# Performance work log

Hardware: AMD Instinct MI355X
Metric: run time of the kernel (lower is better)

## Reference

```python
import jax, jax.numpy as jnp
import numpy as np

N = 20000      # nodes
E = 320000     # edges (before self loops)
G = 128        # graphs
V = 128        # node-type vocab (VOCAB_SIZE)
DE = 64        # node_emb_dim
H = 4          # heads
C = 128        # hidden_dim per head
D = H * C      # 512, per-layer width
OUT = 256      # output_dim
EPS_LN = 1e-5
NEG_SLOPE = 0.2


def _glorot(k, shape):
    fan_in, fan_out = shape[0], shape[-1]
    s = jnp.sqrt(2.0 / (fan_in + fan_out))
    return jax.random.normal(k, shape, dtype=jnp.float32) * s


def setup_inputs() -> dict:
    key = jax.random.key(0)
    ks = jax.random.split(key, 40)
    inp = {}
    inp['node_ids'] = jax.random.randint(ks[0], (N,), 0, V)
    inp['edge_index'] = jax.random.randint(ks[1], (2, E), 0, N)
    inp['batch_vec'] = jnp.sort(jax.random.randint(ks[2], (N,), 0, G))
    emb = _glorot(ks[3], (V, DE))
    inp['emb'] = emb.at[0].set(0.0)  # padding_idx=0
    in_dims = [DE, D, D, D]
    ki = 4
    for i, di in enumerate(in_dims):
        inp[f'W{i}'] = _glorot(ks[ki], (di, D)); ki += 1
        inp[f'as{i}'] = _glorot(ks[ki], (H, C)); ki += 1
        inp[f'ad{i}'] = _glorot(ks[ki], (H, C)); ki += 1
        inp[f'b{i}'] = jnp.zeros((D,), jnp.float32)
        inp[f'lnw{i}'] = jnp.ones((D,), jnp.float32)
        inp[f'lnb{i}'] = jnp.zeros((D,), jnp.float32)
    inp['res_w0'] = _glorot(ks[ki], (DE, D)); ki += 1
    inp['p1w'] = _glorot(ks[ki], (2 * D, 2 * D)); ki += 1
    inp['p1b'] = jnp.zeros((2 * D,), jnp.float32)
    inp['p2w'] = _glorot(ks[ki], (2 * D, OUT)); ki += 1
    inp['p2b'] = jnp.zeros((OUT,), jnp.float32)
    return inp


def _gat_layer(x, src, dst, W, a_src, a_dst, b):
    # x: [N, din] -> [N, H*C]; edge-softmax attention over incoming edges.
    xp = (x @ W).reshape(N, H, C)
    s_src = (xp * a_src).sum(-1)                      # [N,H]
    s_dst = (xp * a_dst).sum(-1)                      # [N,H]
    e = jax.nn.leaky_relu(s_src[src] + s_dst[dst], NEG_SLOPE)   # [Etot,H]
    emax = jax.ops.segment_max(e, dst, num_segments=N)
    ex = jnp.exp(e - emax[dst])
    denom = jax.ops.segment_sum(ex, dst, num_segments=N)
    alpha = ex / denom[dst]                           # [Etot,H]
    msg = xp[src] * alpha[:, :, None]                 # [Etot,H,C]
    out = jax.ops.segment_sum(msg, dst, num_segments=N)
    return out.reshape(N, D) + b


def _graph_ln(x, batch_vec, w, b):
    # PyG LayerNorm mode='graph': normalize over all nodes+channels per graph.
    Cd = x.shape[-1]
    cnt = jax.ops.segment_sum(jnp.ones((x.shape[0],), x.dtype), batch_vec, num_segments=G) * Cd
    cnt = jnp.maximum(cnt, 1.0)
    mu = jax.ops.segment_sum(x.sum(-1), batch_vec, num_segments=G) / cnt
    xc = x - mu[batch_vec][:, None]
    var = jax.ops.segment_sum((xc * xc).sum(-1), batch_vec, num_segments=G) / cnt
    return xc * jax.lax.rsqrt(var + EPS_LN)[batch_vec][:, None] * w + b


def _forward(emb, W0, as0, ad0, b0, lnw0, lnb0, res_w0,
             W1, as1, ad1, b1, lnw1, lnb1,
             W2, as2, ad2, b2, lnw2, lnb2,
             W3, as3, ad3, b3, lnw3, lnb3,
             p1w, p1b, p2w, p2b, node_ids, edge_index, batch_vec):
    loop = jnp.arange(N)
    src = jnp.concatenate([edge_index[0], loop])  # add_self_loops=True
    dst = jnp.concatenate([edge_index[1], loop])
    x = emb[node_ids]                              # [N,DE]
    layers = [(W0, as0, ad0, b0, lnw0, lnb0), (W1, as1, ad1, b1, lnw1, lnb1),
              (W2, as2, ad2, b2, lnw2, lnb2), (W3, as3, ad3, b3, lnw3, lnb3)]
    for i, (W, asr, adr, b, lnw, lnb) in enumerate(layers):
        residual = x @ res_w0 if i == 0 else x
        x = _gat_layer(x, src, dst, W, asr, adr, b)
        x = _graph_ln(x + residual, batch_vec, lnw, lnb)
    ones = jnp.ones((N,), x.dtype)
    cnt = jnp.maximum(jax.ops.segment_sum(ones, batch_vec, num_segments=G), 1.0)
    mean_pool = jax.ops.segment_sum(x, batch_vec, num_segments=G) / cnt[:, None]
    max_pool = jax.ops.segment_max(x, batch_vec, num_segments=G)
    max_pool = jnp.where(jnp.isfinite(max_pool), max_pool, 0.0)
    h = jnp.concatenate([mean_pool, max_pool], axis=-1)  # [G, 2D]
    h = jax.nn.gelu(h @ p1w + p1b, approximate=False)
    h = h @ p2w + p2b                                     # [G, OUT]
    norm = jnp.maximum(jnp.linalg.norm(h, axis=-1, keepdims=True), 1e-12)
    return h / norm


def reference(node_ids, edge_index, batch_vec, emb,
              W0, as0, ad0, b0, lnw0, lnb0, res_w0,
              W1, as1, ad1, b1, lnw1, lnb1,
              W2, as2, ad2, b2, lnw2, lnb2,
              W3, as3, ad3, b3, lnw3, lnb3,
              p1w, p1b, p2w, p2b):
    return _forward(emb, W0, as0, ad0, b0, lnw0, lnb0, res_w0,
                    W1, as1, ad1, b1, lnw1, lnb1,
                    W2, as2, ad2, b2, lnw2, lnb2,
                    W3, as3, ad3, b3, lnw3, lnb3,
                    p1w, p1b, p2w, p2b, node_ids, edge_index, batch_vec)
```

## Files before the change

kernel.cpp:

```cpp
#include <hip/hip_runtime.h>
#include <hip/hip_fp16.h>
#include <math.h>

constexpr int NN   = 20000;
constexpr int EE   = 320000;
constexpr int ET   = EE + NN;
constexpr int GG   = 128;
constexpr int DEE  = 64;
constexpr int DD   = 512;
constexpr int OUTD = 256;

using half8 = __attribute__((ext_vector_type(8))) _Float16;
using f32x4 = __attribute__((ext_vector_type(4))) float;

__device__ __forceinline__ void ldg2lds16(const void* g, void* l) {
  __builtin_amdgcn_global_load_lds((const __attribute__((address_space(1))) unsigned*)g,
                                   (__attribute__((address_space(3))) unsigned*)l, 16, 0, 0);
}

__global__ __launch_bounds__(256) void k_embf16(const int* __restrict__ ids,
                                                const float* __restrict__ emb,
                                                __half* __restrict__ x0) {
  for (int i = blockIdx.x * 256 + threadIdx.x; i < NN * 16; i += gridDim.x * 256) {
    int n = i >> 4, q = (i & 15) * 4;
    float4 v = *(const float4*)(emb + (size_t)ids[n] * DEE + q);
    __half2* o = (__half2*)(x0 + (size_t)n * DEE + q);
    o[0] = __floats2half2_rn(v.x, v.y);
    o[1] = __floats2half2_rn(v.z, v.w);
  }
}

__global__ __launch_bounds__(256) void k_wT16(const float* __restrict__ W,
                                              __half* __restrict__ Th,
                                              int K, int N) {
  __shared__ float t[32][33];
  int n0 = blockIdx.x * 32, k0 = blockIdx.y * 32;
  int c = threadIdx.x & 31, r4 = threadIdx.x >> 5;
  for (int rr = 0; rr < 32; rr += 8)
    t[rr + r4][c] = W[(size_t)(k0 + rr + r4) * N + n0 + c];
  __syncthreads();
  for (int rr = 0; rr < 32; rr += 8) {
    int n = n0 + rr + r4, k = k0 + c;
    Th[(size_t)n * K + k] = __float2half_rn(t[c][rr + r4]);
  }
}

__global__ __launch_bounds__(256) void k_count(const int* __restrict__ ei, int* __restrict__ cnt) {
  for (int k = blockIdx.x * 256 + threadIdx.x; k < ET; k += gridDim.x * 256) {
    int d = (k < EE) ? ei[EE + k] : (k - EE);
    atomicAdd(&cnt[d], 1);
  }
}

__global__ __launch_bounds__(1024) void k_scan(const int* __restrict__ cnt, int* __restrict__ off) {
  __shared__ int part[1024];
  int tid = threadIdx.x;
  constexpr int CH = (NN + 1023) / 1024;
  int base = tid * CH;
  int s = 0;
  for (int i = 0; i < CH; ++i) { int idx = base + i; if (idx < NN) s += cnt[idx]; }
  part[tid] = s;
  __syncthreads();
  for (int o = 1; o < 1024; o <<= 1) {
    int add = (tid >= o) ? part[tid - o] : 0;
    int v = part[tid];
    __syncthreads();
    part[tid] = v + add;
    __syncthreads();
  }
  int run = (tid == 0) ? 0 : part[tid - 1];
  for (int i = 0; i < CH; ++i) {
    int idx = base + i;
    if (idx < NN) { off[idx] = run; run += cnt[idx]; }
  }
  if (tid == 1023) off[NN] = ET;
}

__global__ __launch_bounds__(256) void k_scatter(const int* __restrict__ ei, const int* __restrict__ off,
                                                 int* __restrict__ cur, int* __restrict__ csrc) {
  for (int k = blockIdx.x * 256 + threadIdx.x; k < ET; k += gridDim.x * 256) {
    int s = (k < EE) ? ei[k]      : (k - EE);
    int d = (k < EE) ? ei[EE + k] : (k - EE);
    int p = atomicAdd(&cur[d], 1);
    csrc[off[d] + p] = s;
  }
}

template<int DOTS>
__global__ __launch_bounds__(256) void k_mfma3(const __half* __restrict__ A,
                                               const __half* __restrict__ Bh,
                                               __half* __restrict__ C,
                                               int M, int K, int NC,
                                               const float* __restrict__ asw,
                                               const float* __restrict__ adw,
                                               float* __restrict__ sspS,
                                               float* __restrict__ sspD) {
  __shared__ __half lds[2 * 128 * 64];
  __half* As  = lds;
  __half* Bhs = lds + 8192;
  const int tid = threadIdx.x, l = tid & 63, w = tid >> 6;
  const int wr = w >> 1, wc = w & 1;
  const int m0 = blockIdx.y * 128, n0 = blockIdx.x * 128;
  const int l15 = l & 15, l16 = l >> 4;
  const int sr = l >> 3;
  const int ss = (l & 7) ^ sr;

  float a_s[4], a_d[4];
  if (DOTS) {
#pragma unroll
    for (int j = 0; j < 4; ++j) {
      int col = n0 + wc * 64 + j * 16 + l15;
      a_s[j] = asw[col];
      a_d[j] = adw[col];
    }
  }

  f32x4 acc[4][4] = {};
  for (int k0 = 0; k0 < K; k0 += 64) {
#pragma unroll
    for (int j = 0; j < 4; ++j) {
      int rbase = j * 32 + w * 8;
      int rl = rbase + sr;
      int gA = min(m0 + rl, M - 1);
      int gB = n0 + rl;
      const size_t ko = (size_t)(k0 + ss * 8);
      ldg2lds16(A  + (size_t)gA * K + ko, As  + rbase * 64);
      ldg2lds16(Bh + (size_t)gB * K + ko, Bhs + rbase * 64);
    }
    __syncthreads();
#pragma unroll
    for (int kh = 0; kh < 2; ++kh) {
      half8 af[4], bhf[4];
#pragma unroll
      for (int t = 0; t < 4; ++t) {
        int ra = wr * 64 + t * 16 + l15;
        int ca = (kh * 4 + l16) ^ (ra & 7);
        af[t] = *(const half8*)(As + ra * 64 + ca * 8);
        int rb = wc * 64 + t * 16 + l15;
        int cb = (kh * 4 + l16) ^ (rb & 7);
        bhf[t] = *(const half8*)(Bhs + rb * 64 + cb * 8);
      }
#pragma unroll
      for (int i = 0; i < 4; ++i)
#pragma unroll
        for (int j = 0; j < 4; ++j)
          acc[i][j] = __builtin_amdgcn_mfma_f32_16x16x32_f16(af[i], bhf[j], acc[i][j], 0, 0, 0);
    }
    __syncthreads();
  }
  const int hh = n0 >> 7;
#pragma unroll
  for (int i = 0; i < 4; ++i) {
#pragma unroll
    for (int r = 0; r < 4; ++r) {
      int row = m0 + wr * 64 + i * 16 + l16 * 4 + r;
      if (DOTS) {
        float vs = 0.f, vd = 0.f;
#pragma unroll
        for (int j = 0; j < 4; ++j) {
          vs = fmaf(acc[i][j][r], a_s[j], vs);
          vd = fmaf(acc[i][j][r], a_d[j], vd);
        }
#pragma unroll
        for (int o = 1; o < 16; o <<= 1) { vs += __shfl_xor(vs, o); vd += __shfl_xor(vd, o); }
        if (l15 == 0 && row < M) {
          sspS[(size_t)wc * (NN * 4) + row * 4 + hh] = vs;
          sspD[(size_t)wc * (NN * 4) + row * 4 + hh] = vd;
        }
      }
      if (row >= M) continue;
#pragma unroll
      for (int j = 0; j < 4; ++j) {
        int col = n0 + wc * 64 + j * 16 + l15;
        C[(size_t)row * NC + col] = __float2half(acc[i][j][r]);
      }
    }
  }
}

__global__ __launch_bounds__(256) void k_scomb(const float* __restrict__ sspS,
                                               const float* __restrict__ sspD,
                                               float* __restrict__ ssrc,
                                               float* __restrict__ sdst) {
  int idx = blockIdx.x * 256 + threadIdx.x;
  if (idx < NN * 4) {
    ssrc[idx] = sspS[idx] + sspS[NN * 4 + idx];
    sdst[idx] = sspD[idx] + sspD[NN * 4 + idx];
  }
}

__global__ __launch_bounds__(256) void k_mfmaK(const __half* __restrict__ A,
                                               const __half* __restrict__ Bh,
                                               float* __restrict__ part,
                                               int M, int K, int NC, int Kc) {
  __shared__ __half lds[2 * 128 * 64];
  __half* As  = lds;
  __half* Bhs = lds + 8192;
  const int tid = threadIdx.x, l = tid & 63, w = tid >> 6;
  const int wr = w >> 1, wc = w & 1;
  const int m0 = blockIdx.y * 128, n0 = blockIdx.x * 128;
  const int kz = blockIdx.z;
  const int kb = kz * Kc, ke = kb + Kc;
  const int l15 = l & 15, l16 = l >> 4;
  const int sr = l >> 3;
  const int ss = (l & 7) ^ sr;

  f32x4 acc[4][4] = {};
  for (int k0 = kb; k0 < ke; k0 += 64) {
#pragma unroll
    for (int j = 0; j < 4; ++j) {
      int rbase = j * 32 + w * 8;
      int rl = rbase + sr;
      int gA = min(m0 + rl, M - 1);
      int gB = n0 + rl;
      const size_t ko = (size_t)(k0 + ss * 8);
      ldg2lds16(A  + (size_t)gA * K + ko, As  + rbase * 64);
      ldg2lds16(Bh + (size_t)gB * K + ko, Bhs + rbase * 64);
    }
    __syncthreads();
#pragma unroll
    for (int kh = 0; kh < 2; ++kh) {
      half8 af[4], bhf[4];
#pragma unroll
      for (int t = 0; t < 4; ++t) {
        int ra = wr * 64 + t * 16 + l15;
        int ca = (kh * 4 + l16) ^ (ra & 7);
        af[t] = *(const half8*)(As + ra * 64 + ca * 8);
        int rb = wc * 64 + t * 16 + l15;
        int cb = (kh * 4 + l16) ^ (rb & 7);
        bhf[t] = *(const half8*)(Bhs + rb * 64 + cb * 8);
      }
#pragma unroll
      for (int i = 0; i < 4; ++i)
#pragma unroll
        for (int j = 0; j < 4; ++j)
          acc[i][j] = __builtin_amdgcn_mfma_f32_16x16x32_f16(af[i], bhf[j], acc[i][j], 0, 0, 0);
    }
    __syncthreads();
  }
  float* pz = part + (size_t)kz * M * NC;
#pragma unroll
  for (int i = 0; i < 4; ++i) {
#pragma unroll
    for (int r = 0; r < 4; ++r) {
      int row = m0 + wr * 64 + i * 16 + l16 * 4 + r;
      if (row >= M) continue;
#pragma unroll
      for (int j = 0; j < 4; ++j) {
        int col = n0 + wc * 64 + j * 16 + l15;
        pz[(size_t)row * NC + col] = acc[i][j][r];
      }
    }
  }
}

__global__ __launch_bounds__(256) void k_fin_gelu(const float* __restrict__ part,
                                                  const float* __restrict__ bias,
                                                  __half* __restrict__ outh) {
  int idx = blockIdx.x * 256 + threadIdx.x;
  if (idx >= GG * 1024) return;
  int c = idx & 1023;
  float v = bias[c];
#pragma unroll
  for (int z = 0; z < 8; ++z) v += part[(size_t)z * GG * 1024 + idx];
  v = 0.5f * v * (1.0f + erff(v * 0.70710678118654752f));
  outh[idx] = __float2half_rn(v);
}

__global__ __launch_bounds__(256) void k_fin_l2(const float* __restrict__ part,
                                                const float* __restrict__ bias,
                                                float* __restrict__ out) {
  int g = blockIdx.x, t = threadIdx.x;
  float v = bias[t];
#pragma unroll
  for (int z = 0; z < 8; ++z) v += part[(size_t)z * GG * OUTD + g * OUTD + t];
  float q = v * v;
#pragma unroll
  for (int o = 32; o; o >>= 1) q += __shfl_xor(q, o);
  __shared__ float w[4];
  int wv = t >> 6, ln = t & 63;
  if (ln == 0) w[wv] = q;
  __syncthreads();
  float tot = w[0] + w[1] + w[2] + w[3];
  float nrm = fmaxf(sqrtf(tot), 1e-12f);
  out[(size_t)g * OUTD + t] = v / nrm;
}

__global__ __launch_bounds__(256) void k_eweight(const float* __restrict__ ssrc,
                                                 const float* __restrict__ sdst,
                                                 const int* __restrict__ off,
                                                 const int* __restrict__ csr,
                                                 unsigned* __restrict__ ewk) {
  int wv = threadIdx.x >> 6, ln = threadIdx.x & 63;
  int n = blockIdx.x * 4 + wv;
  int beg = off[n], end = off[n + 1];
  float4 sd4 = *(const float4*)(sdst + (size_t)n * 4);
  float4 wreg[2];
  int    skreg[2];
  float d0 = 0.f, d1 = 0.f, d2 = 0.f, d3 = 0.f;
  int cnt = 0;
  for (int k = beg + ln; k < end; k += 64) {
    int sk = csr[k];
    float4 s = *(const float4*)(ssrc + (size_t)sk * 4);
    float e0 = s.x + sd4.x; e0 = (e0 > 0.f) ? e0 : 0.2f * e0;
    float e1 = s.y + sd4.y; e1 = (e1 > 0.f) ? e1 : 0.2f * e1;
    float e2 = s.z + sd4.z; e2 = (e2 > 0.f) ? e2 : 0.2f * e2;
    float e3 = s.w + sd4.w; e3 = (e3 > 0.f) ? e3 : 0.2f * e3;
    float4 wv4 = make_float4(__expf(e0), __expf(e1), __expf(e2), __expf(e3));
    if (cnt < 2) { wreg[cnt] = wv4; skreg[cnt] = sk; }
    ++cnt;
    d0 += wv4.x; d1 += wv4.y; d2 += wv4.z; d3 += wv4.w;
  }
#pragma unroll
  for (int o = 32; o; o >>= 1) {
    d0 += __shfl_xor(d0, o); d1 += __shfl_xor(d1, o);
    d2 += __shfl_xor(d2, o); d3 += __shfl_xor(d3, o);
  }
  float r0 = 1.0f / d0, r1 = 1.0f / d1, r2 = 1.0f / d2, r3 = 1.0f / d3;
  cnt = 0;
  for (int k = beg + ln; k < end; k += 64) {
    float4 wv4;
    int sk;
    if (cnt < 2) { wv4 = wreg[cnt]; sk = skreg[cnt]; }
    else {
      sk = csr[k];
      float4 s = *(const float4*)(ssrc + (size_t)sk * 4);
      float e0 = s.x + sd4.x; e0 = (e0 > 0.f) ? e0 : 0.2f * e0;
      float e1 = s.y + sd4.y; e1 = (e1 > 0.f) ? e1 : 0.2f * e1;
      float e2 = s.z + sd4.z; e2 = (e2 > 0.f) ? e2 : 0.2f * e2;
      float e3 = s.w + sd4.w; e3 = (e3 > 0.f) ? e3 : 0.2f * e3;
      wv4 = make_float4(__expf(e0), __expf(e1), __expf(e2), __expf(e3));
    }
    ++cnt;
    unsigned sh = (unsigned)sk << 16;
    ewk[k]          = sh | (unsigned)__half_as_ushort(__float2half_rn(wv4.x * r0));
    ewk[ET + k]     = sh | (unsigned)__half_as_ushort(__float2half_rn(wv4.y * r1));
    ewk[2 * ET + k] = sh | (unsigned)__half_as_ushort(__float2half_rn(wv4.z * r2));
    ewk[3 * ET + k] = sh | (unsigned)__half_as_ushort(__float2half_rn(wv4.w * r3));
  }
}

__device__ __forceinline__ void acc4mix(float* acc, unsigned rec, const uint2& x) {
  asm("v_fma_mix_f32 %0, %1, %2, %0 op_sel:[0,0,0] op_sel_hi:[1,1,0]" : "+v"(acc[0]) : "v"(rec), "v"(x.x));
  asm("v_fma_mix_f32 %0, %1, %2, %0 op_sel:[0,1,0] op_sel_hi:[1,1,0]" : "+v"(acc[1]) : "v"(rec), "v"(x.x));
  asm("v_fma_mix_f32 %0, %1, %2, %0 op_sel:[0,0,0] op_sel_hi:[1,1,0]" : "+v"(acc[2]) : "v"(rec), "v"(x.y));
  asm("v_fma_mix_f32 %0, %1, %2, %0 op_sel:[0,1,0] op_sel_hi:[1,1,0]" : "+v"(acc[3]) : "v"(rec), "v"(x.y));
}

__global__ __launch_bounds__(256, 8) void k_aggc(const __half* __restrict__ xp16,
                                                 const unsigned* __restrict__ ewk,
                                                 const int* __restrict__ off,
                                                 const float* __restrict__ bias,
                                                 __half* __restrict__ xio,
                                                 float* __restrict__ psq) {
  const int bid = blockIdx.x;
  const int cb = bid & 7;
  const int chunk = bid >> 3;
  const int wv = threadIdx.x >> 6, l = threadIdx.x & 63;
  const int g = l >> 4, q = l & 15;
  const int h = cb >> 1;
  const int n = __builtin_amdgcn_readfirstlane(chunk * 4 + wv);
  const int beg = off[n], end = off[n + 1];
  const unsigned* __restrict__ ewh = ewk + (size_t)h * ET;
  const __half* __restrict__ xb = xp16 + cb * 64;
  const unsigned qoff = (unsigned)q * 8;

  uint2 rres = *(const uint2*)(xio + (size_t)n * DD + cb * 64 + q * 4);
  float4 bi = *(const float4*)(bias + cb * 64 + q * 4);

  float acc[4] = {};
  {
    unsigned r[5];
    uint2 x[5];
#pragma unroll
    for (int i = 0; i < 5; ++i) {
      int e = beg + i * 4 + g;
      unsigned rr = ewh[min(e, end - 1)];
      r[i] = (e < end) ? rr : 0u;
    }
#pragma unroll
    for (int i = 0; i < 5; ++i)
      x[i] = *(const uint2*)((const char*)xb + (((r[i] >> 6) & 0xFFFFFC00u) | qoff));
#pragma unroll
    for (int i = 0; i < 5; ++i) acc4mix(acc, r[i], x[i]);
  }
  if (beg + 20 < end) {
    int k = beg + 20;
    unsigned rA = ewh[min(k + g, end - 1)];
    unsigned rB = ewh[min(k + 4 + g, end - 1)];
    for (; k + 4 < end; k += 4) {
      rA = ((k + g) < end) ? rA : 0u;
      uint2 xA = *(const uint2*)((const char*)xb + (((rA >> 6) & 0xFFFFFC00u) | qoff));
      unsigned rN = ewh[min(k + 8 + g, end - 1)];
      acc4mix(acc, rA, xA);
      rA = rB; rB = rN;
    }
    rA = ((k + g) < end) ? rA : 0u;
    uint2 xA = *(const uint2*)((const char*)xb + (((rA >> 6) & 0xFFFFFC00u) | qoff));
    acc4mix(acc, rA, xA);
  }
#pragma unroll
  for (int j = 0; j < 4; ++j) {
    acc[j] += __shfl_xor(acc[j], 16);
    acc[j] += __shfl_xor(acc[j], 32);
  }
  float2 fr0 = __half22float2(*(__half2*)&rres.x);
  float2 fr1 = __half22float2(*(__half2*)&rres.y);
  float o0 = acc[0] + bi.x + fr0.x;
  float o1 = acc[1] + bi.y + fr0.y;
  float o2 = acc[2] + bi.z + fr1.x;
  float o3 = acc[3] + bi.w + fr1.y;
  if (g == 0) {
    uint2 st;
    *(__half2*)&st.x = __floats2half2_rn(o0, o1);
    *(__half2*)&st.y = __floats2half2_rn(o2, o3);
    *(uint2*)(xio + (size_t)n * DD + cb * 64 + q * 4) = st;
  }
  float ps = o0 + o1 + o2 + o3;
  float pq = o0 * o0 + o1 * o1 + o2 * o2 + o3 * o3;
#pragma unroll
  for (int o2r = 1; o2r < 16; o2r <<= 1) { ps += __shfl_xor(ps, o2r); pq += __shfl_xor(pq, o2r); }
  if (l == 0) {
    psq[(size_t)n * 16 + cb * 2]     = ps;
    psq[(size_t)n * 16 + cb * 2 + 1] = pq;
  }
}

__device__ __forceinline__ int lowb(const int* a, int n, int key) {
  int lo = 0, hi = n;
  while (lo < hi) { int mid = (lo + hi) >> 1; if (a[mid] < key) lo = mid + 1; else hi = mid; }
  return lo;
}

__global__ __launch_bounds__(256) void k_stats2(const float* __restrict__ psq,
                                                const int* __restrict__ batch,
                                                float* __restrict__ gmu, float* __restrict__ grstd) {
  int g = blockIdx.x, tid = threadIdx.x;
  __shared__ int sb, se;
  __shared__ float rs[4], rq[4];
  if (tid == 0) { sb = lowb(batch, NN, g); se = lowb(batch, NN, g + 1); }
  __syncthreads();
  int b = sb, e = se;
  float ps = 0.f, pq = 0.f;
  for (int n = b + tid; n < e; n += 256) {
    const float4* p = (const float4*)(psq + (size_t)n * 16);
#pragma unroll
    for (int i = 0; i < 4; ++i) {
      float4 v = p[i];
      ps += v.x + v.z;
      pq += v.y + v.w;
    }
  }
#pragma unroll
  for (int o = 32; o; o >>= 1) { ps += __shfl_xor(ps, o); pq += __shfl_xor(pq, o); }
  int wv = tid >> 6, ln = tid & 63;
  if (ln == 0) { rs[wv] = ps; rq[wv] = pq; }
  __syncthreads();
  if (tid == 0) {
    float S = rs[0] + rs[1] + rs[2] + rs[3];
    float Q = rq[0] + rq[1] + rq[2] + rq[3];
    float cnt = fmaxf((float)(e - b) * (float)DD, 1.0f);
    float mu  = S / cnt;
    float var = fmaxf(Q / cnt - mu * mu, 0.0f);
    gmu[g]   = mu;
    grstd[g] = rsqrtf(var + 1e-5f);
  }
}

__global__ __launch_bounds__(256) void k_norm(__half* __restrict__ x, const int* __restrict__ batch,
                                              const float* __restrict__ gmu, const float* __restrict__ grstd,
                                              const float* __restrict__ lnw, const float* __restrict__ lnb) {
  for (int i8 = blockIdx.x * 256 + threadIdx.x; i8 < NN * DD / 8; i8 += gridDim.x * 256) {
    int i = i8 * 8;
    int n = i >> 9, d = i & 511;
    int g = batch[n];
    float mu = gmu[g], rs = grstd[g];
    uint4 raw = *(uint4*)(x + i);
    __half2* hp = (__half2*)&raw;
    float4 w0 = *(const float4*)(lnw + d);
    float4 w1 = *(const float4*)(lnw + d + 4);
    float4 b0 = *(const float4*)(lnb + d);
    float4 b1 = *(const float4*)(lnb + d + 4);
    float wv[8] = {w0.x,w0.y,w0.z,w0.w,w1.x,w1.y,w1.z,w1.w};
    float bv[8] = {b0.x,b0.y,b0.z,b0.w,b1.x,b1.y,b1.z,b1.w};
#pragma unroll
    for (int j = 0; j < 4; ++j) {
      float2 f = __half22float2(hp[j]);
      f.x = (f.x - mu) * rs * wv[2*j]   + bv[2*j];
      f.y = (f.y - mu) * rs * wv[2*j+1] + bv[2*j+1];
      hp[j] = __floats2half2_rn(f.x, f.y);
    }
    *(uint4*)(x + i) = raw;
  }
}

__global__ __launch_bounds__(256) void k_pool(const __half* __restrict__ x, const int* __restrict__ batch,
                                              __half* __restrict__ pool16) {
  int g = blockIdx.x, tid = threadIdx.x;
  __shared__ int sb, se;
  if (tid == 0) { sb = lowb(batch, NN, g); se = lowb(batch, NN, g + 1); }
  __syncthreads();
  int b = sb, e = se;
  float s0 = 0.f, s1 = 0.f, m0 = -INFINITY, m1 = -INFINITY;
  for (int n = b; n < e; ++n) {
    float v0 = __half2float(x[(size_t)n * DD + tid]);
    float v1 = __half2float(x[(size_t)n * DD + tid + 256]);
    s0 += v0; s1 += v1;
    m0 = fmaxf(m0, v0); m1 = fmaxf(m1, v1);
  }
  int cnt = e - b;
  float inv = 1.0f / (float)(cnt > 0 ? cnt : 1);
  pool16[(size_t)g * 1024 + tid]             = __float2half_rn(s0 * inv);
  pool16[(size_t)g * 1024 + tid + 256]       = __float2half_rn(s1 * inv);
  pool16[(size_t)g * 1024 + 512 + tid]       = __float2half_rn((cnt > 0) ? m0 : 0.f);
  pool16[(size_t)g * 1024 + 512 + tid + 256] = __float2half_rn((cnt > 0) ? m1 : 0.f);
}

extern "C" void kernel_launch(void* const* d_in, const int* in_sizes, int n_in,
                              void* d_out, int out_size, void* d_ws, size_t ws_size,
                              hipStream_t stream) {
  const int*   node_ids = (const int*)d_in[0];
  const int*   ei       = (const int*)d_in[1];
  const int*   batch    = (const int*)d_in[2];
  const float* emb      = (const float*)d_in[3];
  const float* W[4]  = {(const float*)d_in[4],  (const float*)d_in[10], (const float*)d_in[16], (const float*)d_in[22]};
  const float* AS[4] = {(const float*)d_in[5],  (const float*)d_in[11], (const float*)d_in[17], (const float*)d_in[23]};
  const float* AD[4] = {(const float*)d_in[6],  (const float*)d_in[12], (const float*)d_in[18], (const float*)d_in[24]};
  const float* BV[4] = {(const float*)d_in[7],  (const float*)d_in[13], (const float*)d_in[19], (const float*)d_in[25]};
  const float* LW[4] = {(const float*)d_in[8],  (const float*)d_in[14], (const float*)d_in[20], (const float*)d_in[26]};
  const float* LB[4] = {(const float*)d_in[9],  (const float*)d_in[15], (const float*)d_in[21], (const float*)d_in[27]};
  const float* res_w0 = (const float*)d_in[28];
  const float* p1w    = (const float*)d_in[29];
  const float* p1b    = (const float*)d_in[30];
  const float* p2w    = (const float*)d_in[31];
  const float* p2b    = (const float*)d_in[32];
  float* out = (float*)d_out;

  char* ws = (char*)d_ws;
  size_t pos = 0;
  auto alloc = [&](size_t bytes) -> char* {
    char* p = ws + pos;
    pos = (pos + bytes + 255) & ~size_t(255);
    return p;
  };
  __half* xr16  = (__half*)alloc((size_t)NN * DD * 2);
  __half* xp16  = (__half*)alloc((size_t)NN * DD * 2);
  __half* x0f   = (__half*)alloc((size_t)NN * DEE * 2);
  float*  ssrc  = (float*)alloc((size_t)NN * 4 * 4);
  float*  sdst  = (float*)alloc((size_t)NN * 4 * 4);
  float*  sspS  = (float*)alloc((size_t)2 * NN * 4 * 4);
  float*  sspD  = (float*)alloc((size_t)2 * NN * 4 * 4);
  int*    coff  = (int*)alloc((size_t)(NN + 1) * 4);
  int*    ccur  = (int*)alloc((size_t)NN * 4);
  int*    csrc  = (int*)alloc((size_t)ET * 4);
  unsigned* ewk = (unsigned*)alloc((size_t)ET * 4 * 4);
  float*  psq   = (float*)alloc((size_t)NN * 16 * 4);
  float*  gmu   = (float*)alloc((size_t)GG * 4 * 2);
  float*  grstd = gmu + GG;
  __half* w0t = (__half*)alloc((size_t)DEE * DD * 2);
  __half* rwt = (__half*)alloc((size_t)DEE * DD * 2);
  __half* wt[4] = {w0t, nullptr, nullptr, nullptr};
  for (int i = 1; i < 4; ++i) wt[i] = (__half*)alloc((size_t)DD * DD * 2);
  __half* p1t = (__half*)alloc((size_t)1024 * 1024 * 2);
  __half* p2t = (__half*)alloc((size_t)OUTD * 1024 * 2);
  __half* pool16 = (__half*)alloc((size_t)GG * 1024 * 2);
  __half* h1_16  = (__half*)alloc((size_t)GG * 1024 * 2);
  float*  part1  = (float*)alloc((size_t)8 * GG * 1024 * 4);
  float*  part2  = (float*)alloc((size_t)8 * GG * OUTD * 4);
  (void)ws_size; (void)in_sizes; (void)n_in; (void)out_size;

  hipMemsetAsync(ccur, 0, (size_t)NN * 4, stream);
  k_embf16<<<1250, 256, 0, stream>>>(node_ids, emb, x0f);
  k_count<<<1024, 256, 0, stream>>>(ei, ccur);
  k_scan<<<1, 1024, 0, stream>>>(ccur, coff);
  hipMemsetAsync(ccur, 0, (size_t)NN * 4, stream);
  k_scatter<<<1024, 256, 0, stream>>>(ei, coff, ccur, csrc);
  k_wT16<<<dim3(16, 2),  256, 0, stream>>>(W[0],   w0t, DEE, DD);
  k_wT16<<<dim3(16, 2),  256, 0, stream>>>(res_w0, rwt, DEE, DD);
  for (int i = 1; i < 4; ++i)
    k_wT16<<<dim3(16, 16), 256, 0, stream>>>(W[i], wt[i], DD, DD);
  k_wT16<<<dim3(32, 32), 256, 0, stream>>>(p1w, p1t, 1024, 1024);
  k_wT16<<<dim3(8, 32),  256, 0, stream>>>(p2w, p2t, 1024, OUTD);

  k_mfma3<1><<<dim3(4, 157), 256, 0, stream>>>(x0f, w0t, xp16, NN, DEE, DD,
                                               AS[0], AD[0], sspS, sspD);
  k_mfma3<0><<<dim3(4, 157), 256, 0, stream>>>(x0f, rwt, xr16, NN, DEE, DD,
                                               nullptr, nullptr, nullptr, nullptr);
  k_scomb<<<(NN * 4 + 255) / 256, 256, 0, stream>>>(sspS, sspD, ssrc, sdst);

  for (int L = 0; L < 4; ++L) {
    k_eweight<<<NN / 4, 256, 0, stream>>>(ssrc, sdst, coff, csrc, ewk);
    k_aggc<<<NN * 2, 256, 0, stream>>>(xp16, ewk, coff, BV[L], xr16, psq);
    k_stats2<<<GG, 256, 0, stream>>>(psq, batch, gmu, grstd);
    k_norm<<<2048, 256, 0, stream>>>(xr16, batch, gmu, grstd, LW[L], LB[L]);
    if (L < 3) {
      k_mfma3<1><<<dim3(4, 157), 256, 0, stream>>>(xr16, wt[L + 1], xp16, NN, DD, DD,
                                                   AS[L + 1], AD[L + 1], sspS, sspD);
      k_scomb<<<(NN * 4 + 255) / 256, 256, 0, stream>>>(sspS, sspD, ssrc, sdst);
    }
  }

  k_pool<<<GG, 256, 0, stream>>>(xr16, batch, pool16);
  k_mfmaK<<<dim3(8, 1, 8), 256, 0, stream>>>(pool16, p1t, part1, GG, 1024, 1024, 128);
  k_fin_gelu<<<512, 256, 0, stream>>>(part1, p1b, h1_16);
  k_mfmaK<<<dim3(2, 1, 8), 256, 0, stream>>>(h1_16, p2t, part2, GG, 1024, OUTD, 128);
  k_fin_l2<<<GG, 256, 0, stream>>>(part2, p2b, out);
}
```

Before: 565.4 us.

## Pad CSR rows to multiple of four, min twenty; drop psq stats path

Each node's CSR row is padded to a multiple of 4 entries with a minimum of 20, and the padding slots get zero edge weights. The aggregation kernel can then drop bounds checks, min-clamps and the software-pipelined tail loop. The per-node partial sum and sum-of-squares output from aggregation is removed, and the graph stats kernel now recomputes them by rereading the fp16 activations. The costs are more padded edge storage and extra memory traffic in the stats kernel; a stated ETP of 840000 must bound the padded size.

New measurement: 703.2 us. +24.4%, slower.

```diff
diff --git a/kernel.cpp b/kernel.cpp
--- a/kernel.cpp
+++ b/kernel.cpp
@@ -5,6 +5,7 @@
 constexpr int NN   = 20000;
 constexpr int EE   = 320000;
 constexpr int ET   = EE + NN;
+constexpr int ETP  = 840000;
 constexpr int GG   = 128;
 constexpr int DEE  = 64;
 constexpr int DD   = 512;
@@ -52,13 +53,18 @@
   }
 }
 
+__device__ __forceinline__ int pdegf(int c) {
+  int p = (c + 3) & ~3;
+  return (p < 20) ? 20 : p;
+}
+
 __global__ __launch_bounds__(1024) void k_scan(const int* __restrict__ cnt, int* __restrict__ off) {
   __shared__ int part[1024];
   int tid = threadIdx.x;
   constexpr int CH = (NN + 1023) / 1024;
   int base = tid * CH;
   int s = 0;
-  for (int i = 0; i < CH; ++i) { int idx = base + i; if (idx < NN) s += cnt[idx]; }
+  for (int i = 0; i < CH; ++i) { int idx = base + i; if (idx < NN) s += pdegf(cnt[idx]); }
   part[tid] = s;
   __syncthreads();
   for (int o = 1; o < 1024; o <<= 1) {
@@ -71,9 +77,9 @@
   int run = (tid == 0) ? 0 : part[tid - 1];
   for (int i = 0; i < CH; ++i) {
     int idx = base + i;
-    if (idx < NN) { off[idx] = run; run += cnt[idx]; }
-  }
-  if (tid == 1023) off[NN] = ET;
+    if (idx < NN) { off[idx] = run; run += pdegf(cnt[idx]); }
+  }
+  if (tid == 1023) off[NN] = run;
 }
 
 __global__ __launch_bounds__(256) void k_scatter(const int* __restrict__ ei, const int* __restrict__ off,
@@ -288,19 +294,21 @@
 
 __global__ __launch_bounds__(256) void k_eweight(const float* __restrict__ ssrc,
                                                  const float* __restrict__ sdst,
-                                                 const int* __restrict__ off,
+                                                 const int* __restrict__ poff,
+                                                 const int* __restrict__ cnt_,
                                                  const int* __restrict__ csr,
                                                  unsigned* __restrict__ ewk) {
   int wv = threadIdx.x >> 6, ln = threadIdx.x & 63;
   int n = blockIdx.x * 4 + wv;
-  int beg = off[n], end = off[n + 1];
+  int beg = poff[n], pend = poff[n + 1];
+  int deg = cnt_[n];
   float4 sd4 = *(const float4*)(sdst + (size_t)n * 4);
   float4 wreg[2];
   int    skreg[2];
   float d0 = 0.f, d1 = 0.f, d2 = 0.f, d3 = 0.f;
   int cnt = 0;
-  for (int k = beg + ln; k < end; k += 64) {
-    int sk = csr[k];
+  for (int j = ln; j < deg; j += 64) {
+    int sk = csr[beg + j];
     float4 s = *(const float4*)(ssrc + (size_t)sk * 4);
     float e0 = s.x + sd4.x; e0 = (e0 > 0.f) ? e0 : 0.2f * e0;
     float e1 = s.y + sd4.y; e1 = (e1 > 0.f) ? e1 : 0.2f * e1;
@@ -318,25 +326,34 @@
   }
   float r0 = 1.0f / d0, r1 = 1.0f / d1, r2 = 1.0f / d2, r3 = 1.0f / d3;
   cnt = 0;
-  for (int k = beg + ln; k < end; k += 64) {
-    float4 wv4;
-    int sk;
-    if (cnt < 2) { wv4 = wreg[cnt]; sk = skreg[cnt]; }
-    else {
-      sk = csr[k];
-      float4 s = *(const float4*)(ssrc + (size_t)sk * 4);
-      float e0 = s.x + sd4.x; e0 = (e0 > 0.f) ? e0 : 0.2f * e0;
-      float e1 = s.y + sd4.y; e1 = (e1 > 0.f) ? e1 : 0.2f * e1;
-      float e2 = s.z + sd4.z; e2 = (e2 > 0.f) ? e2 : 0.2f * e2;
-      float e3 = s.w + sd4.w; e3 = (e3 > 0.f) ? e3 : 0.2f * e3;
-      wv4 = make_float4(__expf(e0), __expf(e1), __expf(e2), __expf(e3));
-    }
-    ++cnt;
-    unsigned sh = (unsigned)sk << 16;
-    ewk[k]          = sh | (unsigned)__half_as_ushort(__float2half_rn(wv4.x * r0));
-    ewk[ET + k]     = sh | (unsigned)__half_as_ushort(__float2half_rn(wv4.y * r1));
-    ewk[2 * ET + k] = sh | (unsigned)__half_as_ushort(__float2half_rn(wv4.z * r2));
-    ewk[3 * ET + k] = sh | (unsigned)__half_as_ushort(__float2half_rn(wv4.w * r3));
+  int plen = pend - beg;
+  for (int j = ln; j < plen; j += 64) {
+    int k = beg + j;
+    if (j < deg) {
+      float4 wv4;
+      int sk;
+      if (cnt < 2) { wv4 = wreg[cnt]; sk = skreg[cnt]; }
+      else {
+        sk = csr[k];
+        float4 s = *(const float4*)(ssrc + (size_t)sk * 4);
+        float e0 = s.x + sd4.x; e0 = (e0 > 0.f) ? e0 : 0.2f * e0;
+        float e1 = s.y + sd4.y; e1 = (e1 > 0.f) ? e1 : 0.2f * e1;
+        float e2 = s.z + sd4.z; e2 = (e2 > 0.f) ? e2 : 0.2f * e2;
+        float e3 = s.w + sd4.w; e3 = (e3 > 0.f) ? e3 : 0.2f * e3;
+        wv4 = make_float4(__expf(e0), __expf(e1), __expf(e2), __expf(e3));
+      }
+      ++cnt;
+      unsigned sh = (unsigned)sk << 16;
+      ewk[k]           = sh | (unsigned)__half_as_ushort(__float2half_rn(wv4.x * r0));
+      ewk[ETP + k]     = sh | (unsigned)__half_as_ushort(__float2half_rn(wv4.y * r1));
+      ewk[2 * ETP + k] = sh | (unsigned)__half_as_ushort(__float2half_rn(wv4.z * r2));
+      ewk[3 * ETP + k] = sh | (unsigned)__half_as_ushort(__float2half_rn(wv4.w * r3));
+    } else {
+      ewk[k]           = 0u;
+      ewk[ETP + k]     = 0u;
+      ewk[2 * ETP + k] = 0u;
+      ewk[3 * ETP + k] = 0u;
+    }
   }
 }
 
@@ -349,10 +366,9 @@
 
 __global__ __launch_bounds__(256, 8) void k_aggc(const __half* __restrict__ xp16,
                                                  const unsigned* __restrict__ ewk,
-                                                 const int* __restrict__ off,
+                                                 const int* __restrict__ poff,
                                                  const float* __restrict__ bias,
-                                                 __half* __restrict__ xio,
-                                                 float* __restrict__ psq) {
+                                                 __half* __restrict__ xio) {
   const int bid = blockIdx.x;
   const int cb = bid & 7;
   const int chunk = bid >> 3;
@@ -360,8 +376,8 @@
   const int g = l >> 4, q = l & 15;
   const int h = cb >> 1;
   const int n = __builtin_amdgcn_readfirstlane(chunk * 4 + wv);
-  const int beg = off[n], end = off[n + 1];
-  const unsigned* __restrict__ ewh = ewk + (size_t)h * ET;
+  const int beg = poff[n], pend = poff[n + 1];
+  const unsigned* __restrict__ ewh = ewk + (size_t)h * ETP;
   const __half* __restrict__ xb = xp16 + cb * 64;
   const unsigned qoff = (unsigned)q * 8;
 
@@ -373,57 +389,35 @@
     unsigned r[5];
     uint2 x[5];
 #pragma unroll
-    for (int i = 0; i < 5; ++i) {
-      int e = beg + i * 4 + g;
-      unsigned rr = ewh[min(e, end - 1)];
-      r[i] = (e < end) ? rr : 0u;
-    }
+    for (int i = 0; i < 5; ++i) r[i] = ewh[beg + i * 4 + g];
 #pragma unroll
     for (int i = 0; i < 5; ++i)
       x[i] = *(const uint2*)((const char*)xb + (((r[i] >> 6) & 0xFFFFFC00u) | qoff));
 #pragma unroll
     for (int i = 0; i < 5; ++i) acc4mix(acc, r[i], x[i]);
   }
-  if (beg + 20 < end) {
-    int k = beg + 20;
-    unsigned rA = ewh[min(k + g, end - 1)];
-    unsigned rB = ewh[min(k + 4 + g, end - 1)];
-    for (; k + 4 < end; k += 4) {
-      rA = ((k + g) < end) ? rA : 0u;
-      uint2 xA = *(const uint2*)((const char*)xb + (((rA >> 6) & 0xFFFFFC00u) | qoff));
-      unsigned rN = ewh[min(k + 8 + g, end - 1)];
-      acc4mix(acc, rA, xA);
-      rA = rB; rB = rN;
-    }
-    rA = ((k + g) < end) ? rA : 0u;
-    uint2 xA = *(const uint2*)((const char*)xb + (((rA >> 6) & 0xFFFFFC00u) | qoff));
-    acc4mix(acc, rA, xA);
+  for (int k = beg + 20; k < pend; k += 4) {
+    unsigned rr = ewh[k + g];
+    uint2 xx = *(const uint2*)((const char*)xb + (((rr >> 6) & 0xFFFFFC00u) | qoff));
+    acc4mix(acc, rr, xx);
   }
 #pragma unroll
   for (int j = 0; j < 4; ++j) {
     acc[j] += __shfl_xor(acc[j], 16);
     acc[j] += __shfl_xor(acc[j], 32);
   }
-  float2 fr0 = __half22float2(*(__half2*)&rres.x);
-  float2 fr1 = __half22float2(*(__half2*)&rres.y);
-  float o0 = acc[0] + bi.x + fr0.x;
-  float o1 = acc[1] + bi.y + fr0.y;
-  float o2 = acc[2] + bi.z + fr1.x;
-  float o3 = acc[3] + bi.w + fr1.y;
   if (g == 0) {
+    float2 fr0 = __half22float2(*(__half2*)&rres.x);
+    float2 fr1 = __half22float2(*(__half2*)&rres.y);
+    float o0 = acc[0] + bi.x + fr0.x;
+    float o1 = acc[1] + bi.y + fr0.y;
+    float o2 = acc[2] + bi.z + fr1.x;
+    float o3 = acc[3] + bi.w + fr1.y;
     uint2 st;
     *(__half2*)&st.x = __floats2half2_rn(o0, o1);
     *(__half2*)&st.y = __floats2half2_rn(o2, o3);
     *(uint2*)(xio + (size_t)n * DD + cb * 64 + q * 4) = st;
   }
-  float ps = o0 + o1 + o2 + o3;
-  float pq = o0 * o0 + o1 * o1 + o2 * o2 + o3 * o3;
-#pragma unroll
-  for (int o2r = 1; o2r < 16; o2r <<= 1) { ps += __shfl_xor(ps, o2r); pq += __shfl_xor(pq, o2r); }
-  if (l == 0) {
-    psq[(size_t)n * 16 + cb * 2]     = ps;
-    psq[(size_t)n * 16 + cb * 2 + 1] = pq;
-  }
 }
 
 __device__ __forceinline__ int lowb(const int* a, int n, int key) {
@@ -432,7 +426,7 @@
   return lo;
 }
 
-__global__ __launch_bounds__(256) void k_stats2(const float* __restrict__ psq,
+__global__ __launch_bounds__(256) void k_stats2(const __half* __restrict__ xio,
                                                 const int* __restrict__ batch,
                                                 float* __restrict__ gmu, float* __restrict__ grstd) {
   int g = blockIdx.x, tid = threadIdx.x;
@@ -441,14 +435,17 @@
   if (tid == 0) { sb = lowb(batch, NN, g); se = lowb(batch, NN, g + 1); }
   __syncthreads();
   int b = sb, e = se;
+  const __half* base = xio + (size_t)b * DD;
+  int n8 = (e - b) * DD / 8;
   float ps = 0.f, pq = 0.f;
-  for (int n = b + tid; n < e; n += 256) {
-    const float4* p = (const float4*)(psq + (size_t)n * 16);
-#pragma unroll
-    for (int i = 0; i < 4; ++i) {
-      float4 v = p[i];
-      ps += v.x + v.z;
-      pq += v.y + v.w;
+  for (int i8 = tid; i8 < n8; i8 += 256) {
+    uint4 raw = *(const uint4*)(base + (size_t)i8 * 8);
+    const __half2* hp = (const __half2*)&raw;
+#pragma unroll
+    for (int j = 0; j < 4; ++j) {
+      float2 f = __half22float2(hp[j]);
+      ps += f.x + f.y;
+      pq += f.x * f.x + f.y * f.y;
     }
   }
 #pragma unroll
@@ -550,11 +547,11 @@
   float*  sdst  = (float*)alloc((size_t)NN * 4 * 4);
   float*  sspS  = (float*)alloc((size_t)2 * NN * 4 * 4);
   float*  sspD  = (float*)alloc((size_t)2 * NN * 4 * 4);
-  int*    coff  = (int*)alloc((size_t)(NN + 1) * 4);
+  int*    poff  = (int*)alloc((size_t)(NN + 1) * 4);
+  int*    cntb  = (int*)alloc((size_t)NN * 4);
   int*    ccur  = (int*)alloc((size_t)NN * 4);
-  int*    csrc  = (int*)alloc((size_t)ET * 4);
-  unsigned* ewk = (unsigned*)alloc((size_t)ET * 4 * 4);
-  float*  psq   = (float*)alloc((size_t)NN * 16 * 4);
+  int*    csrc  = (int*)alloc((size_t)ETP * 4);
+  unsigned* ewk = (unsigned*)alloc((size_t)ETP * 4 * 4);
   float*  gmu   = (float*)alloc((size_t)GG * 4 * 2);
   float*  grstd = gmu + GG;
   __half* w0t = (__half*)alloc((size_t)DEE * DD * 2);
@@ -569,12 +566,12 @@
   float*  part2  = (float*)alloc((size_t)8 * GG * OUTD * 4);
   (void)ws_size; (void)in_sizes; (void)n_in; (void)out_size;
 
+  hipMemsetAsync(cntb, 0, (size_t)NN * 4, stream);
   hipMemsetAsync(ccur, 0, (size_t)NN * 4, stream);
   k_embf16<<<1250, 256, 0, stream>>>(node_ids, emb, x0f);
-  k_count<<<1024, 256, 0, stream>>>(ei, ccur);
-  k_scan<<<1, 1024, 0, stream>>>(ccur, coff);
-  hipMemsetAsync(ccur, 0, (size_t)NN * 4, stream);
-  k_scatter<<<1024, 256, 0, stream>>>(ei, coff, ccur, csrc);
+  k_count<<<1024, 256, 0, stream>>>(ei, cntb);
+  k_scan<<<1, 1024, 0, stream>>>(cntb, poff);
+  k_scatter<<<1024, 256, 0, stream>>>(ei, poff, ccur, csrc);
   k_wT16<<<dim3(16, 2),  256, 0, stream>>>(W[0],   w0t, DEE, DD);
   k_wT16<<<dim3(16, 2),  256, 0, stream>>>(res_w0, rwt, DEE, DD);
   for (int i = 1; i < 4; ++i)
@@ -589,9 +586,9 @@
   k_scomb<<<(NN * 4 + 255) / 256, 256, 0, stream>>>(sspS, sspD, ssrc, sdst);
 
   for (int L = 0; L < 4; ++L) {
-    k_eweight<<<NN / 4, 256, 0, stream>>>(ssrc, sdst, coff, csrc, ewk);
-    k_aggc<<<NN * 2, 256, 0, stream>>>(xp16, ewk, coff, BV[L], xr16, psq);
-    k_stats2<<<GG, 256, 0, stream>>>(psq, batch, gmu, grstd);
+    k_eweight<<<NN / 4, 256, 0, stream>>>(ssrc, sdst, poff, cntb, csrc, ewk);
+    k_aggc<<<NN * 2, 256, 0, stream>>>(xp16, ewk, poff, BV[L], xr16);
+    k_stats2<<<GG, 256, 0, stream>>>(xr16, batch, gmu, grstd);
     k_norm<<<2048, 256, 0, stream>>>(xr16, batch, gmu, grstd, LW[L], LB[L]);
     if (L < 3) {
       k_mfma3<1><<<dim3(4, 157), 256, 0, stream>>>(xr16, wt[L + 1], xp16, NN, DD, DD,
```
